# Performance work log

Hardware: AMD Instinct MI355X
Metric: run time of the kernel (lower is better)

Reference implementation:

```python
import jax, jax.numpy as jnp
import numpy as np

H = 4096          # hidden_size
NH = 32           # num_attention_heads
NKV = 2           # multi_query_group_num (kv heads)
HD = 128          # kv_channels / head_dim
RD = 64           # rotary_dim = head_dim * rotary_percent(0.5)
T = 2048          # total tokens (single prefill sequence)
EPS = 1e-5        # layernorm_epsilon
ROPE_BASE = 10000.0


def setup_inputs() -> dict:
    key = jax.random.key(0)
    k0, k1, k2, k3 = jax.random.split(key, 4)
    qkv_out = (NH + 2 * NKV) * HD  # 4608
    return {
        "positions": jnp.arange(T, dtype=jnp.int32),
        "hidden_states": jax.random.normal(k0, (T, H), jnp.float32),
        "w_qkv": jax.random.normal(k1, (qkv_out, H), jnp.float32) * 0.02,
        "b_qkv": jax.random.normal(k2, (qkv_out,), jnp.float32) * 0.02,
        "w_dense": jax.random.normal(k3, (H, NH * HD), jnp.float32) * 0.02,
        "q_ln_w": jnp.ones((HD,), jnp.float32),
        "k_ln_w": jnp.ones((HD,), jnp.float32),
    }


def _rmsnorm(x, w):
    # per-head RMSNorm over head_dim
    return x * jax.lax.rsqrt(jnp.mean(x * x, axis=-1, keepdims=True) + EPS) * w


def _rope(x, positions):
    # partial rotary (first RD dims), interleaved GPT-J style (is_neox_style=False)
    inv_freq = 1.0 / (ROPE_BASE ** (jnp.arange(0, RD, 2, dtype=jnp.float32) / RD))
    ang = positions.astype(jnp.float32)[:, None] * inv_freq      # [T, RD//2]
    cos = jnp.cos(ang)[:, None, :]                               # [T, 1, RD//2]
    sin = jnp.sin(ang)[:, None, :]
    x_rot, x_pass = x[..., :RD], x[..., RD:]
    x1 = x_rot[..., 0::2]
    x2 = x_rot[..., 1::2]
    r1 = x1 * cos - x2 * sin
    r2 = x2 * cos + x1 * sin
    x_rot = jnp.stack([r1, r2], axis=-1).reshape(x.shape[:-1] + (RD,))
    return jnp.concatenate([x_rot, x_pass], axis=-1)


def reference(positions, hidden_states, w_qkv, b_qkv, w_dense, q_ln_w, k_ln_w):
    qkv = hidden_states @ w_qkv.T + b_qkv                        # [T, 4608]
    q_size, kv_size = NH * HD, NKV * HD
    q = qkv[:, :q_size].reshape(T, NH, HD)
    k = qkv[:, q_size:q_size + kv_size].reshape(T, NKV, HD)
    v = qkv[:, q_size + kv_size:].reshape(T, NKV, HD)
    # optional qk layernorm (RMSNorm since config.rmsnorm)
    q = _rmsnorm(q, q_ln_w)
    k = _rmsnorm(k, k_ln_w)
    # rotary embedding
    q = _rope(q, positions)
    k = _rope(k, positions)
    # GQA: expand kv heads to query heads
    group = NH // NKV
    k_exp = jnp.repeat(k, group, axis=1)                         # [T, NH, HD]
    v_exp = jnp.repeat(v, group, axis=1)
    scale = HD ** -0.5
    scores = jnp.einsum("thd,shd->hts", q, k_exp) * scale        # [NH, T, T]
    causal = jnp.tril(jnp.ones((T, T), dtype=bool))
    scores = jnp.where(causal[None, :, :], scores, jnp.finfo(scores.dtype).min)
    attn = jax.nn.softmax(scores, axis=-1)
    out = jnp.einsum("hts,shd->thd", attn, v_exp).reshape(T, NH * HD)
    return out @ w_dense.T                                       # [T, H]
```

## Files before the change

kernel.cpp:

```cpp
#include <hip/hip_runtime.h>
#include <cstdint>
#include <cstddef>

typedef short short4v __attribute__((ext_vector_type(4)));
typedef short short8v __attribute__((ext_vector_type(8)));
typedef float f32x4   __attribute__((ext_vector_type(4)));

#define T_LEN  2048
#define HDIM   4096
#define NHEADS 32
#define HEADD  128
#define QKVN   4608

static __device__ __forceinline__ short f2bf(float f) {
  __bf16 h = (__bf16)f;
  return __builtin_bit_cast(short, h);
}
static __device__ __forceinline__ float bf2f(short u) {
  return __builtin_bit_cast(float, ((unsigned int)(unsigned short)u) << 16);
}

static __device__ __forceinline__ void gload_lds16(const void* g, void* l) {
  __builtin_amdgcn_global_load_lds((const __attribute__((address_space(1))) void*)g,
                                   (__attribute__((address_space(3))) void*)l,
                                   16, 0, 0);
}

__global__ void cast_f32_to_bf16(const float* __restrict__ in, short* __restrict__ out, int n4) {
  int idx = blockIdx.x * blockDim.x + threadIdx.x;
  int stride = gridDim.x * blockDim.x;
  const float4* in4 = (const float4*)in;
  short4v* out4 = (short4v*)out;
  for (int i = idx; i < n4; i += stride) {
    float4 v = in4[i];
    short4v o;
    o[0] = f2bf(v.x); o[1] = f2bf(v.y); o[2] = f2bf(v.z); o[3] = f2bf(v.w);
    out4[i] = o;
  }
}

template <int OUT_BF16>
__global__ __launch_bounds__(256, 2) void gemm_bt(
    const short* __restrict__ A,
    const short* __restrict__ B,
    const float* __restrict__ bias,
    void* __restrict__ Cout,
    int M, int N, int K)
{
  __shared__ short sA[2][128 * 32];
  __shared__ short sB[2][128 * 32];
  const int tid  = threadIdx.x;
  const int lane = tid & 63;
  const int wv   = tid >> 6;
  const int wr   = wv >> 1;
  const int wc   = wv & 1;

  const int nwg  = gridDim.x * gridDim.y;
  int wgid = blockIdx.y * gridDim.x + blockIdx.x;
  wgid = (wgid & 7) * (nwg >> 3) + (wgid >> 3);
  const int bn0 = (wgid / gridDim.y) * 128;
  const int bm0 = (wgid % gridDim.y) * 128;

  const int row0 = tid >> 2;
  const int kc0  = (tid & 3) * 8;
  const int row1 = row0 + 64;
  const short* gA0 = A + (size_t)(bm0 + row0) * K + kc0;
  const short* gA1 = A + (size_t)(bm0 + row1) * K + kc0;
  const short* gB0 = B + (size_t)(bn0 + row0) * K + kc0;
  const short* gB1 = B + (size_t)(bn0 + row1) * K + kc0;

  const int fr = lane & 15;
  const int fk = (lane >> 4) * 8;

  auto STAGE = [&](int b, int kt) {
    short* lA = &sA[b][0] + wv * 64 * 8;
    short* lB = &sB[b][0] + wv * 64 * 8;
    gload_lds16(gA0 + kt, lA);
    gload_lds16(gA1 + kt, lA + 256 * 8);
    gload_lds16(gB0 + kt, lB);
    gload_lds16(gB1 + kt, lB + 256 * 8);
  };

  f32x4 zero = {0.f, 0.f, 0.f, 0.f};
  f32x4 acc[4][4];
#pragma unroll
  for (int m = 0; m < 4; m++)
#pragma unroll
    for (int n = 0; n < 4; n++) acc[m][n] = zero;

  int cur = 0;
  STAGE(0, 0);
  __syncthreads();

  for (int kt = 0; kt < K; kt += 32) {
    if (kt + 32 < K) STAGE(cur ^ 1, kt + 32);
    const short* aB = &sA[cur][0];
    const short* bB = &sB[cur][0];
    short8v af[4], bfr[4];
#pragma unroll
    for (int m = 0; m < 4; m++)
      af[m] = *(const short8v*)(aB + (wr * 64 + m * 16 + fr) * 32 + fk);
#pragma unroll
    for (int n = 0; n < 4; n++)
      bfr[n] = *(const short8v*)(bB + (wc * 64 + n * 16 + fr) * 32 + fk);
#pragma unroll
    for (int m = 0; m < 4; m++)
#pragma unroll
      for (int n = 0; n < 4; n++)
        acc[m][n] = __builtin_amdgcn_mfma_f32_16x16x32_bf16(af[m], bfr[n], acc[m][n], 0, 0, 0);
    __syncthreads();
    cur ^= 1;
  }

  const int rg = (lane >> 4) * 4;
#pragma unroll
  for (int m = 0; m < 4; m++) {
#pragma unroll
    for (int n = 0; n < 4; n++) {
      const int gcol = bn0 + wc * 64 + n * 16 + fr;
      const float bv = bias ? bias[gcol] : 0.0f;
#pragma unroll
      for (int j = 0; j < 4; j++) {
        const int grow = bm0 + wr * 64 + m * 16 + rg + j;
        const float v = acc[m][n][j] + bv;
        if (OUT_BF16)
          ((short*)Cout)[(size_t)grow * N + gcol] = f2bf(v);
        else
          ((float*)Cout)[(size_t)grow * N + gcol] = v;
      }
    }
  }
}

__global__ __launch_bounds__(64) void qkv_post_kernel(
    const short* __restrict__ qkvb,
    const int*   __restrict__ positions,
    const float* __restrict__ q_ln,
    const float* __restrict__ k_ln,
    short* __restrict__ Qb,
    short* __restrict__ Kb,
    short* __restrict__ Vt)
{
  const int t = blockIdx.x;
  const int h = blockIdx.y;
  const int lane = threadIdx.x;
  const unsigned int pk =
      ((const unsigned int*)(qkvb + (size_t)t * QKVN + h * HEADD))[lane];
  float x = bf2f((short)(pk & 0xffffu));
  float y = bf2f((short)(pk >> 16));

  if (h >= 34) {
    const int hv = h - 34;
    short* dst = Vt + ((size_t)hv * HEADD + 2 * lane) * T_LEN + t;
    dst[0]     = f2bf(x);
    dst[T_LEN] = f2bf(y);
    return;
  }

  float ss = x * x + y * y;
#pragma unroll
  for (int d = 32; d > 0; d >>= 1) ss += __shfl_xor(ss, d);
  const float r = rsqrtf(ss * (1.0f / 128.0f) + 1e-5f);
  const float* lnw = (h < 32) ? q_ln : k_ln;
  x = x * r * lnw[2 * lane];
  y = y * r * lnw[2 * lane + 1];

  if (lane < 32) {
    const float pos = (float)positions[t];
    const float ang = pos * powf(10000.0f, -(float)lane * (1.0f / 32.0f));
    const float c = cosf(ang), s = sinf(ang);
    const float r1 = x * c - y * s;
    const float r2 = y * c + x * s;
    x = r1; y = r2;
  }

  short* dst = (h < 32) ? (Qb + ((size_t)h * T_LEN + t) * HEADD + 2 * lane)
                        : (Kb + ((size_t)(h - 32) * T_LEN + t) * HEADD + 2 * lane);
  dst[0] = f2bf(x);
  dst[1] = f2bf(y);
}

__global__ __launch_bounds__(256, 2) void attn_kernel(
    const short* __restrict__ Qb,
    const short* __restrict__ Kb,
    const short* __restrict__ Vt,
    short* __restrict__ attn_out)
{
  __shared__ short Ks[2][64 * 128];
  __shared__ short Vs[2][128 * 64];
  __shared__ short pbuf[4][32 * 64];
  const int blk  = gridDim.x - 1 - blockIdx.x;
  const int h    = blockIdx.y;
  const int hkv  = h >> 4;
  const int tid  = threadIdx.x;
  const int lane = tid & 63;
  const int wv   = tid >> 6;
  const int B0   = blk * 128;
  const int qrow0 = B0 + wv * 32;
  const int fr = lane & 15;
  const int fk = (lane >> 4) * 8;
  const int fkb = (lane >> 4) << 4;
  const int rg = (lane >> 4) * 4;
  const int swz = (fr & 7) << 4;

  const short* Kh = Kb + (size_t)hkv * T_LEN * HEADD;
  const short* Vh = Vt + (size_t)hkv * HEADD * T_LEN;

  short8v qf[2][4];
#pragma unroll
  for (int g = 0; g < 2; g++) {
    const short* Qrow = Qb + ((size_t)h * T_LEN + qrow0 + g * 16 + fr) * HEADD + fk;
#pragma unroll
    for (int d0 = 0; d0 < 4; d0++) qf[g][d0] = *(const short8v*)(Qrow + d0 * 32);
  }

  float mrow[2][4], lrow[2][4];
#pragma unroll
  for (int g = 0; g < 2; g++)
#pragma unroll
    for (int j = 0; j < 4; j++) { mrow[g][j] = -1e30f; lrow[g][j] = 0.f; }
  f32x4 zero = {0.f, 0.f, 0.f, 0.f};
  f32x4 o[2][8];
#pragma unroll
  for (int g = 0; g < 2; g++)
#pragma unroll
    for (int d = 0; d < 8; d++) o[g][d] = zero;

  char* pb = (char*)&pbuf[wv][0];
  const float scale = 0.08838834764831845f;
  const int nt = 2 * blk + 2;

  auto STAGE = [&](int b, int t) {
    const int s0 = t * 64;
#pragma unroll
    for (int i = 0; i < 4; i++) {
      const int c    = i * 256 + tid;
      const int row  = c >> 4;
      const int colb = (c & 15) << 4;
      const int scol = (colb ^ ((row & 7) << 4)) >> 1;
      gload_lds16(Kh + (size_t)(s0 + row) * HEADD + scol,
                  (char*)&Ks[b][0] + (size_t)(i * 256 + wv * 64) * 16);
    }
#pragma unroll
    for (int i = 0; i < 4; i++) {
      const int c    = i * 256 + tid;
      const int row  = c >> 3;
      const int colb = (c & 7) << 4;
      const int scol = (colb ^ ((row & 7) << 4)) >> 1;
      gload_lds16(Vh + (size_t)row * T_LEN + s0 + scol,
                  (char*)&Vs[b][0] + (size_t)(i * 256 + wv * 64) * 16);
    }
  };

  int cur = 0;
  STAGE(0, 0);
  __syncthreads();

  for (int t = 0; t < nt; ++t) {
    if (t + 1 < nt) STAGE(cur ^ 1, t + 1);
    const int s0 = t * 64;
    const char* KsB = (const char*)&Ks[cur][0];
    const char* VsB = (const char*)&Vs[cur][0];

    float scv[2][4][4];
#pragma unroll
    for (int sub = 0; sub < 4; sub++) {
      const char* Kbase = KsB + (sub * 16 + fr) * 256;
      f32x4 a0 = zero, a1 = zero;
#pragma unroll
      for (int d0 = 0; d0 < 4; d0++) {
        short8v kf = *(const short8v*)(Kbase + ((d0 * 64 + fkb) ^ swz));
        a0 = __builtin_amdgcn_mfma_f32_16x16x32_bf16(qf[0][d0], kf, a0, 0, 0, 0);
        a1 = __builtin_amdgcn_mfma_f32_16x16x32_bf16(qf[1][d0], kf, a1, 0, 0, 0);
      }
#pragma unroll
      for (int j = 0; j < 4; j++) {
        scv[0][sub][j] = a0[j] * scale;
        scv[1][sub][j] = a1[j] * scale;
      }
    }
    if (t >= nt - 2) {
#pragma unroll
      for (int g = 0; g < 2; g++)
#pragma unroll
        for (int sub = 0; sub < 4; sub++) {
          const int colp = s0 + sub * 16 + fr;
#pragma unroll
          for (int j = 0; j < 4; j++)
            if (colp > qrow0 + g * 16 + rg + j) scv[g][sub][j] = -1e30f;
        }
    }
    float pmax[2][4];
#pragma unroll
    for (int g = 0; g < 2; g++)
#pragma unroll
      for (int j = 0; j < 4; j++)
        pmax[g][j] = fmaxf(fmaxf(scv[g][0][j], scv[g][1][j]),
                           fmaxf(scv[g][2][j], scv[g][3][j]));
    float growth = -1e30f;
#pragma unroll
    for (int g = 0; g < 2; g++)
#pragma unroll
      for (int j = 0; j < 4; j++) growth = fmaxf(growth, pmax[g][j] - mrow[g][j]);
    if (!__all(growth <= 8.0f)) {
#pragma unroll
      for (int g = 0; g < 2; g++)
#pragma unroll
        for (int j = 0; j < 4; j++) {
          float mx = pmax[g][j];
#pragma unroll
          for (int d = 1; d < 16; d <<= 1) mx = fmaxf(mx, __shfl_xor(mx, d));
          const float mn = fmaxf(mrow[g][j], mx);
          const float c  = __expf(mrow[g][j] - mn);
          mrow[g][j] = mn;
          lrow[g][j] *= c;
#pragma unroll
          for (int df = 0; df < 8; df++) o[g][df][j] *= c;
        }
    }
#pragma unroll
    for (int g = 0; g < 2; g++)
#pragma unroll
      for (int j = 0; j < 4; j++) {
        const int prow = g * 16 + rg + j;
        char* prb = pb + prow * 128;
        const int rswz = ((rg + j) & 7) << 4;
        float ps = 0.f;
#pragma unroll
        for (int sub = 0; sub < 4; sub++) {
          const float p = __expf(scv[g][sub][j] - mrow[g][j]);
          ps += p;
          *(short*)(prb + ((((sub * 16 + fr) << 1)) ^ rswz)) = f2bf(p);
        }
        lrow[g][j] += ps;
      }
    asm volatile("" ::: "memory");
    short8v pf[2][2];
#pragma unroll
    for (int g = 0; g < 2; g++)
#pragma unroll
      for (int ks = 0; ks < 2; ks++)
        pf[g][ks] = *(const short8v*)(pb + (g * 16 + fr) * 128 + ((ks * 64 + fkb) ^ swz));
#pragma unroll
    for (int df = 0; df < 8; df++) {
      const char* Vbase = VsB + (df * 16 + fr) * 128;
      short8v vf0 = *(const short8v*)(Vbase + ((0 + fkb) ^ swz));
      short8v vf1 = *(const short8v*)(Vbase + ((64 + fkb) ^ swz));
      o[0][df] = __builtin_amdgcn_mfma_f32_16x16x32_bf16(pf[0][0], vf0, o[0][df], 0, 0, 0);
      o[0][df] = __builtin_amdgcn_mfma_f32_16x16x32_bf16(pf[0][1], vf1, o[0][df], 0, 0, 0);
      o[1][df] = __builtin_amdgcn_mfma_f32_16x16x32_bf16(pf[1][0], vf0, o[1][df], 0, 0, 0);
      o[1][df] = __builtin_amdgcn_mfma_f32_16x16x32_bf16(pf[1][1], vf1, o[1][df], 0, 0, 0);
    }
    __syncthreads();
    cur ^= 1;
  }

#pragma unroll
  for (int g = 0; g < 2; g++)
#pragma unroll
    for (int j = 0; j < 4; j++) {
#pragma unroll
      for (int d = 1; d < 16; d <<= 1) lrow[g][j] += __shfl_xor(lrow[g][j], d);
    }
#pragma unroll
  for (int g = 0; g < 2; g++)
#pragma unroll
    for (int df = 0; df < 8; df++)
#pragma unroll
      for (int j = 0; j < 4; j++) {
        const float v = o[g][df][j] / lrow[g][j];
        attn_out[(size_t)(qrow0 + g * 16 + rg + j) * HDIM + h * HEADD + df * 16 + fr] = f2bf(v);
      }
}

extern "C" void kernel_launch(void* const* d_in, const int* in_sizes, int n_in,
                              void* d_out, int out_size, void* d_ws, size_t ws_size,
                              hipStream_t stream) {
  (void)out_size; (void)ws_size;
  int ip = 0, ih = 1, iwq = 2, ib = 3, iwd = 4, il0 = 5, il1 = 6;
  if (n_in == 7) {
    int p = -1, hh = -1, wq = -1, b = -1, wd = -1, l0 = -1, l1 = -1, ok = 1;
    for (int i = 0; i < 7; i++) {
      switch (in_sizes[i]) {
        case 2048:     p  = i; break;
        case 8388608:  hh = i; break;
        case 18874368: wq = i; break;
        case 4608:     b  = i; break;
        case 16777216: wd = i; break;
        case 128:      if (l0 < 0) l0 = i; else l1 = i; break;
        default:       ok = 0; break;
      }
    }
    if (ok && p >= 0 && hh >= 0 && wq >= 0 && b >= 0 && wd >= 0 && l0 >= 0 && l1 >= 0) {
      ip = p; ih = hh; iwq = wq; ib = b; iwd = wd; il0 = l0; il1 = l1;
    }
  }

  const int*   positions = (const int*)d_in[ip];
  const float* hidden    = (const float*)d_in[ih];
  const float* w_qkv     = (const float*)d_in[iwq];
  const float* b_qkv     = (const float*)d_in[ib];
  const float* w_dense   = (const float*)d_in[iwd];
  const float* q_ln      = (const float*)d_in[il0];
  const float* k_ln      = (const float*)d_in[il1];

  char* ws = (char*)d_ws;
  short* Ahs   = (short*)(ws + 0);
  short* Qb    = (short*)(ws + 0);
  short* Wqkv  = (short*)(ws + (size_t)16777216);
  short* Kb    = (short*)(ws + (size_t)16777216);
  short* Vt    = (short*)(ws + (size_t)17825792);
  short* Wd    = (short*)(ws + (size_t)18874368);
  short* qkvb  = (short*)(ws + (size_t)54525952);
  short* attnb = (short*)(ws + (size_t)54525952);

  cast_f32_to_bf16<<<dim3(1024), dim3(256), 0, stream>>>(hidden, Ahs, (T_LEN * HDIM) / 4);
  cast_f32_to_bf16<<<dim3(2048), dim3(256), 0, stream>>>(w_qkv, Wqkv, (QKVN * HDIM) / 4);
  gemm_bt<1><<<dim3(QKVN / 128, T_LEN / 128), dim3(256), 0, stream>>>(
      Ahs, Wqkv, b_qkv, (void*)qkvb, T_LEN, QKVN, HDIM);
  qkv_post_kernel<<<dim3(T_LEN, 36), dim3(64), 0, stream>>>(
      qkvb, positions, q_ln, k_ln, Qb, Kb, Vt);
  cast_f32_to_bf16<<<dim3(2048), dim3(256), 0, stream>>>(w_dense, Wd, (HDIM * HDIM) / 4);
  attn_kernel<<<dim3(16, NHEADS), dim3(256), 0, stream>>>(Qb, Kb, Vt, attnb);
  gemm_bt<0><<<dim3(HDIM / 128, T_LEN / 128), dim3(256), 0, stream>>>(
      attnb, Wd, nullptr, d_out, T_LEN, HDIM, HDIM);
}
```

Baseline: 355.6 us.

## Merge cast kernels, fold dense-weight cast into attention, batch qkv_post heads, add setprio

Merges the two f32-to-bf16 casts into one launch, and moves the w_dense cast into the start of the attention kernel so it no longer needs its own launch. qkv_post_kernel now runs four heads per 256-thread block to cut the block count. s_setprio is raised around the MFMA sections of attention so waves doing matrix work are scheduled first. Fusing the cast means every attention block first streams part of the 64MB weight before it starts attention work, which can delay attention.

```diff
diff --git a/kernel.cpp b/kernel.cpp
--- a/kernel.cpp
+++ b/kernel.cpp
@@ -26,16 +26,18 @@
                                    16, 0, 0);
 }
 
-__global__ void cast_f32_to_bf16(const float* __restrict__ in, short* __restrict__ out, int n4) {
+__global__ void cast_pair(const float* __restrict__ a, short* __restrict__ oa, int na4,
+                          const float* __restrict__ b, short* __restrict__ ob, int nb4) {
   int idx = blockIdx.x * blockDim.x + threadIdx.x;
   int stride = gridDim.x * blockDim.x;
-  const float4* in4 = (const float4*)in;
-  short4v* out4 = (short4v*)out;
-  for (int i = idx; i < n4; i += stride) {
-    float4 v = in4[i];
+  const int ntot = na4 + nb4;
+  for (int i = idx; i < ntot; i += stride) {
+    const float4* src = (i < na4) ? ((const float4*)a + i) : ((const float4*)b + (i - na4));
+    short4v* dst      = (i < na4) ? ((short4v*)oa + i)     : ((short4v*)ob + (i - na4));
+    float4 v = *src;
     short4v o;
     o[0] = f2bf(v.x); o[1] = f2bf(v.y); o[2] = f2bf(v.z); o[3] = f2bf(v.w);
-    out4[i] = o;
+    *dst = o;
   }
 }
 
@@ -132,7 +134,7 @@
   }
 }
 
-__global__ __launch_bounds__(64) void qkv_post_kernel(
+__global__ __launch_bounds__(256) void qkv_post_kernel(
     const short* __restrict__ qkvb,
     const int*   __restrict__ positions,
     const float* __restrict__ q_ln,
@@ -142,8 +144,8 @@
     short* __restrict__ Vt)
 {
   const int t = blockIdx.x;
-  const int h = blockIdx.y;
-  const int lane = threadIdx.x;
+  const int h = blockIdx.y * 4 + (threadIdx.x >> 6);
+  const int lane = threadIdx.x & 63;
   const unsigned int pk =
       ((const unsigned int*)(qkvb + (size_t)t * QKVN + h * HEADD))[lane];
   float x = bf2f((short)(pk & 0xffffu));
@@ -184,15 +186,31 @@
     const short* __restrict__ Qb,
     const short* __restrict__ Kb,
     const short* __restrict__ Vt,
-    short* __restrict__ attn_out)
+    short* __restrict__ attn_out,
+    const float* __restrict__ wd_src,
+    short* __restrict__ wd_dst)
 {
   __shared__ short Ks[2][64 * 128];
   __shared__ short Vs[2][128 * 64];
   __shared__ short pbuf[4][32 * 64];
+  const int tid  = threadIdx.x;
+
+  {
+    const int bid = blockIdx.y * gridDim.x + blockIdx.x;
+    const int stride = gridDim.x * gridDim.y * 256;
+    const float4* s4 = (const float4*)wd_src;
+    short4v* d4 = (short4v*)wd_dst;
+    for (int i = bid * 256 + tid; i < (HDIM * HDIM) / 4; i += stride) {
+      float4 v = s4[i];
+      short4v o;
+      o[0] = f2bf(v.x); o[1] = f2bf(v.y); o[2] = f2bf(v.z); o[3] = f2bf(v.w);
+      d4[i] = o;
+    }
+  }
+
   const int blk  = gridDim.x - 1 - blockIdx.x;
   const int h    = blockIdx.y;
   const int hkv  = h >> 4;
-  const int tid  = threadIdx.x;
   const int lane = tid & 63;
   const int wv   = tid >> 6;
   const int B0   = blk * 128;
@@ -263,6 +281,7 @@
     const char* VsB = (const char*)&Vs[cur][0];
 
     float scv[2][4][4];
+    __builtin_amdgcn_s_setprio(1);
 #pragma unroll
     for (int sub = 0; sub < 4; sub++) {
       const char* Kbase = KsB + (sub * 16 + fr) * 256;
@@ -279,6 +298,7 @@
         scv[1][sub][j] = a1[j] * scale;
       }
     }
+    __builtin_amdgcn_s_setprio(0);
     if (t >= nt - 2) {
 #pragma unroll
       for (int g = 0; g < 2; g++)
@@ -341,6 +361,7 @@
 #pragma unroll
       for (int ks = 0; ks < 2; ks++)
         pf[g][ks] = *(const short8v*)(pb + (g * 16 + fr) * 128 + ((ks * 64 + fkb) ^ swz));
+    __builtin_amdgcn_s_setprio(1);
 #pragma unroll
     for (int df = 0; df < 8; df++) {
       const char* Vbase = VsB + (df * 16 + fr) * 128;
@@ -351,6 +372,7 @@
       o[1][df] = __builtin_amdgcn_mfma_f32_16x16x32_bf16(pf[1][0], vf0, o[1][df], 0, 0, 0);
       o[1][df] = __builtin_amdgcn_mfma_f32_16x16x32_bf16(pf[1][1], vf1, o[1][df], 0, 0, 0);
     }
+    __builtin_amdgcn_s_setprio(0);
     __syncthreads();
     cur ^= 1;
   }
@@ -414,14 +436,14 @@
   short* qkvb  = (short*)(ws + (size_t)54525952);
   short* attnb = (short*)(ws + (size_t)54525952);
 
-  cast_f32_to_bf16<<<dim3(1024), dim3(256), 0, stream>>>(hidden, Ahs, (T_LEN * HDIM) / 4);
-  cast_f32_to_bf16<<<dim3(2048), dim3(256), 0, stream>>>(w_qkv, Wqkv, (QKVN * HDIM) / 4);
+  cast_pair<<<dim3(3072), dim3(256), 0, stream>>>(
+      hidden, Ahs, (T_LEN * HDIM) / 4, w_qkv, Wqkv, (QKVN * HDIM) / 4);
   gemm_bt<1><<<dim3(QKVN / 128, T_LEN / 128), dim3(256), 0, stream>>>(
       Ahs, Wqkv, b_qkv, (void*)qkvb, T_LEN, QKVN, HDIM);
-  qkv_post_kernel<<<dim3(T_LEN, 36), dim3(64), 0, stream>>>(
+  qkv_post_kernel<<<dim3(T_LEN, 9), dim3(256), 0, stream>>>(
       qkvb, positions, q_ln, k_ln, Qb, Kb, Vt);
-  cast_f32_to_bf16<<<dim3(2048), dim3(256), 0, stream>>>(w_dense, Wd, (HDIM * HDIM) / 4);
-  attn_kernel<<<dim3(16, NHEADS), dim3(256), 0, stream>>>(Qb, Kb, Vt, attnb);
+  attn_kernel<<<dim3(16, NHEADS), dim3(256), 0, stream>>>(
+      Qb, Kb, Vt, attnb, w_dense, Wd);
   gemm_bt<0><<<dim3(HDIM / 128, T_LEN / 128), dim3(256), 0, stream>>>(
       attnb, Wd, nullptr, d_out, T_LEN, HDIM, HDIM);
 }
```

Result: no change. 362.4 us (+1.9%).
